# Performance work log

Measured on AMD Instinct MI355X. Metric: run time of the kernel, lower is better.

Reference implementation:

```python
import jax, jax.numpy as jnp
import numpy as np

B, S, E, H, FF = 4, 2048, 1024, 16, 4096
DK = E // H
EPS = 1e-5


def setup_inputs() -> dict:
    key = jax.random.key(0)
    ks = jax.random.split(key, 16)
    sc = 0.02
    return {
        "x": jax.random.normal(ks[0], (B, S, E), jnp.float32),
        "Wq": jax.random.normal(ks[1], (E, E), jnp.float32) * sc,
        "Wk": jax.random.normal(ks[2], (E, E), jnp.float32) * sc,
        "Wv": jax.random.normal(ks[3], (E, E), jnp.float32) * sc,
        "Wo": jax.random.normal(ks[4], (E, E), jnp.float32) * sc,
        "theta": jax.random.normal(ks[5], (DK,), jnp.float32),
        "Wcq": jax.random.normal(ks[6], (E, E), jnp.float32) * sc,
        "ln1_g": jnp.ones((E,), jnp.float32),
        "ln1_b": jnp.zeros((E,), jnp.float32),
        "W1": jax.random.normal(ks[7], (E, FF), jnp.float32) * sc,
        "b1": jnp.zeros((FF,), jnp.float32),
        "W2": jax.random.normal(ks[8], (FF, E), jnp.float32) * sc,
        "b2": jnp.zeros((E,), jnp.float32),
        "ln2_g": jnp.ones((E,), jnp.float32),
        "ln2_b": jnp.zeros((E,), jnp.float32),
    }


def _layernorm(x, g, b):
    mu = jnp.mean(x, axis=-1, keepdims=True)
    var = jnp.mean(jnp.square(x - mu), axis=-1, keepdims=True)
    return (x - mu) * jax.lax.rsqrt(var + EPS) * g + b


def reference(x, Wq, Wk, Wv, Wo, theta, Wcq, ln1_g, ln1_b, W1, b1, W2, b2, ln2_g, ln2_b):
    mix = 0.5
    # classical multi-head attention
    def heads(t):  # [B,S,E] -> [B,H,S,DK]
        return t.reshape(B, S, H, DK).transpose(0, 2, 1, 3)
    q = heads(x @ Wq)
    k = heads(x @ Wk)
    v = heads(x @ Wv)
    scores = jnp.einsum("bhqd,bhkd->bhqk", q, k) / jnp.sqrt(jnp.float32(DK))
    attn = jax.nn.softmax(scores, axis=-1)
    ctx = jnp.einsum("bhqk,bhkd->bhqd", attn, v)
    ctx = ctx.transpose(0, 2, 1, 3).reshape(B, S, E)
    classical = ctx @ Wo
    # quantum heads: RX(x)RX(theta)|0>, <Z> = cos(x + theta), same theta shared per head
    qh = jnp.cos(x.reshape(B, S, H, DK) + theta)  # broadcast over wires
    quantum = qh.reshape(B, S, E) @ Wcq
    attn_out = mix * classical + (1.0 - mix) * quantum
    x1 = _layernorm(x + attn_out, ln1_g, ln1_b)
    ffn = jax.nn.relu(x1 @ W1 + b1) @ W2 + b2
    return _layernorm(x1 + ffn, ln2_g, ln2_b)
```

## Files before the change

kernel.cpp:

```cpp
#include <hip/hip_runtime.h>
#include <hip/hip_bf16.h>

typedef __bf16 bf16_t;
typedef bf16_t bf16x8 __attribute__((ext_vector_type(8)));
typedef bf16_t bf16x4v __attribute__((ext_vector_type(4)));
typedef float f32x4 __attribute__((ext_vector_type(4)));
typedef unsigned u32x4 __attribute__((ext_vector_type(4)));

static constexpr int EE = 1024;
static constexpr int SS = 2048;
static constexpr int DK = 64;
static constexpr float QSCALE = 0.125f * 1.44269504f;

__device__ __forceinline__ void gload_lds16(const void* g, void* l) {
  __builtin_amdgcn_global_load_lds(
      (__attribute__((address_space(1))) void*)g,
      (__attribute__((address_space(3))) void*)l, 16, 0, 0);
}

__device__ __forceinline__ f32x4 mfma16(bf16x8 a, bf16x8 b, f32x4 c) {
  return __builtin_amdgcn_mfma_f32_16x16x32_bf16(a, b, c, 0, 0, 0);
}

template<int OFF>
__device__ __forceinline__ bf16x4v tr8(unsigned va) {
  bf16x4v d;
  asm volatile("ds_read_b64_tr_b16 %0, %1 offset:%c2"
               : "=v"(d) : "v"(va), "i"(OFF));
  return d;
}

__global__ void __launch_bounds__(256) prep_x_kernel(
    const float* __restrict__ x, const float* __restrict__ theta,
    bf16_t* __restrict__ xbf, bf16_t* __restrict__ A2)
{
  const long t = (long)blockIdx.x * 256 + threadIdx.x;
  const long e0 = t * 8;
  const int col = (int)(e0 & (EE - 1));
  const long row = e0 >> 10;
  const float4 v0 = *(const float4*)&x[e0];
  const float4 v1 = *(const float4*)&x[e0 + 4];
  float xs[8] = {v0.x, v0.y, v0.z, v0.w, v1.x, v1.y, v1.z, v1.w};
  const int d0 = col & (DK - 1);
  bf16x8 xb, qb;
#pragma unroll
  for (int j = 0; j < 8; ++j) {
    xb[j] = (bf16_t)xs[j];
    qb[j] = (bf16_t)__cosf(xs[j] + theta[d0 + j]);
  }
  *(bf16x8*)&xbf[e0] = xb;
  *(bf16x8*)&A2[row * 2048 + EE + col] = qb;
}

__global__ void __launch_bounds__(256) transpose_all_kernel(
    const float* __restrict__ Wq, const float* __restrict__ Wk,
    const float* __restrict__ Wv, const float* __restrict__ Wo,
    const float* __restrict__ Wcq, const float* __restrict__ W1,
    const float* __restrict__ W2,
    bf16_t* __restrict__ BtQKV, bf16_t* __restrict__ Bt2,
    bf16_t* __restrict__ BtW1, bf16_t* __restrict__ BtW2)
{
  const int bid = blockIdx.x;
  const float* src; bf16_t* dst; int N; long dstride, dcol0; int bx, by;
  if (bid < 5120) {
    const int seg = bid >> 10, r = bid & 1023;
    bx = r & 31; by = r >> 5; N = 1024;
    if      (seg == 0) { src = Wq;  dst = BtQKV;               dstride = 1024; dcol0 = 0; }
    else if (seg == 1) { src = Wk;  dst = BtQKV + 1024 * 1024; dstride = 1024; dcol0 = 0; }
    else if (seg == 2) { src = Wv;  dst = BtQKV + 2048 * 1024; dstride = 1024; dcol0 = 0; }
    else if (seg == 3) { src = Wo;  dst = Bt2;                 dstride = 2048; dcol0 = 0; }
    else               { src = Wcq; dst = Bt2;                 dstride = 2048; dcol0 = 1024; }
  } else if (bid < 9216) {
    const int r = bid - 5120;
    src = W1; dst = BtW1; N = 4096; dstride = 1024; dcol0 = 0;
    bx = r & 127; by = r >> 7;
  } else {
    const int r = bid - 9216;
    src = W2; dst = BtW2; N = 1024; dstride = 4096; dcol0 = 0;
    bx = r & 31; by = r >> 5;
  }
  __shared__ float tile[32][33];
  const int tx = threadIdx.x, ty = threadIdx.y;
  const long n0 = (long)bx * 32, k0 = (long)by * 32;
#pragma unroll
  for (int j = 0; j < 4; ++j)
    tile[ty + j * 8][tx] = src[(k0 + ty + j * 8) * N + n0 + tx];
  __syncthreads();
#pragma unroll
  for (int j = 0; j < 4; ++j)
    dst[(n0 + ty + j * 8) * dstride + dcol0 + k0 + tx] = (bf16_t)tile[tx][ty + j * 8];
}

template<int MODE, int TN>
__global__ void __launch_bounds__(512, 2) gemm256(
    const bf16_t* __restrict__ A, const bf16_t* __restrict__ Bt,
    void* __restrict__ C, int M, int N, int K,
    const float* __restrict__ aux1, const bf16_t* __restrict__ aux2)
{
  constexpr int MB  = (TN == 256) ? 8 : 4;
  constexpr int MBH = MB / 2;
  constexpr int NB  = 4;
  __shared__ bf16_t As[4][256 * 32];
  __shared__ bf16_t Bs[4][TN * 32];
  const int tid = threadIdx.x;
  const int lane = tid & 63, wid = tid >> 6;
  const int wr = (TN == 256) ? (wid >> 2) : (wid >> 1);
  const int wc = (TN == 256) ? (wid & 3) : (wid & 1);
  const int lr = lane & 15, lk = lane >> 4;
  const int gx = gridDim.x;
  const int nwg = gx * gridDim.y;
  const int bid = blockIdx.y * gx + blockIdx.x;
  const int swz = (bid & 7) * (nwg >> 3) + (bid >> 3);
  const long m0 = (long)(swz / gx) * 256;
  const long n0 = (long)(swz % gx) * TN;

  const int rql = lane >> 2;
  const int sl  = lane & 3;
  const int rA0 = wid * 32 + rql, rA1 = wid * 32 + 16 + rql;
  const bf16_t* sA0 = &A [(m0 + rA0) * K + 8 * (sl ^ ((rA0 >> 1) & 3))];
  const bf16_t* sA1 = &A [(m0 + rA1) * K + 8 * (sl ^ ((rA1 >> 1) & 3))];
  const int rB0 = (TN == 256) ? (wid * 32 + rql) : (wid * 16 + rql);
  const int rB1 = wid * 32 + 16 + rql;
  const bf16_t* sB0 = &Bt[(n0 + rB0) * K + 8 * (sl ^ ((rB0 >> 1) & 3))];
  const bf16_t* sB1 = &Bt[(n0 + rB1) * K + 8 * (sl ^ ((rB1 >> 1) & 3))];
  const int loA = wid * 1024;
  const int loB = (TN == 256) ? wid * 1024 : wid * 512;

  f32x4 acc[MB][NB] = {};
  const int NKT = K / 32;

  auto stA = [&](int t) {
    const int s = t & 3;
    gload_lds16(sA0 + (long)t * 32, &As[s][loA]);
    gload_lds16(sA1 + (long)t * 32, &As[s][loA + 512]);
  };
  auto stB = [&](int t) {
    const int s = t & 3;
    gload_lds16(sB0 + (long)t * 32, &Bs[s][loB]);
    if constexpr (TN == 256)
      gload_lds16(sB1 + (long)t * 32, &Bs[s][loB + 512]);
  };

  stA(0); stB(0); stA(1); stB(1); stA(2); stB(2);
  if constexpr (TN == 256) { asm volatile("s_waitcnt vmcnt(8)" ::: "memory"); }
  else                     { asm volatile("s_waitcnt vmcnt(6)" ::: "memory"); }
  __builtin_amdgcn_s_barrier();

  for (int t = 0; t < NKT; ++t) {
    const int s = t & 3;
    bf16x8 bfr[NB], af1[MBH], af2[MBH];
#pragma unroll
    for (int nb = 0; nb < NB; ++nb) {
      const int rw = wc * 64 + nb * 16 + lr;
      bfr[nb] = *(const bf16x8*)&Bs[s][rw * 32 + (lk ^ ((rw >> 1) & 3)) * 8];
    }
#pragma unroll
    for (int mb = 0; mb < MBH; ++mb) {
      const int rw = wr * (MB * 16) + mb * 16 + lr;
      af1[mb] = *(const bf16x8*)&As[s][rw * 32 + (lk ^ ((rw >> 1) & 3)) * 8];
    }
    __builtin_amdgcn_sched_barrier(0);
#pragma unroll
    for (int mb = 0; mb < MBH; ++mb) {
      const int rw = wr * (MB * 16) + (MBH + mb) * 16 + lr;
      af2[mb] = *(const bf16x8*)&As[s][rw * 32 + (lk ^ ((rw >> 1) & 3)) * 8];
    }
    if (t + 3 < NKT) { stA(t + 3); stB(t + 3); }
    if constexpr (MBH == 4) { asm volatile("s_waitcnt lgkmcnt(4)" ::: "memory"); }
    else                    { asm volatile("s_waitcnt lgkmcnt(2)" ::: "memory"); }
    __builtin_amdgcn_sched_barrier(0);
    __builtin_amdgcn_s_setprio(1);
#pragma unroll
    for (int mb = 0; mb < MBH; ++mb)
#pragma unroll
      for (int nb = 0; nb < NB; ++nb)
        acc[mb][nb] = mfma16(af1[mb], bfr[nb], acc[mb][nb]);
    __builtin_amdgcn_s_setprio(0);
    asm volatile("s_waitcnt lgkmcnt(0)" ::: "memory");
    __builtin_amdgcn_sched_barrier(0);
    __builtin_amdgcn_s_setprio(1);
#pragma unroll
    for (int mb = 0; mb < MBH; ++mb)
#pragma unroll
      for (int nb = 0; nb < NB; ++nb)
        acc[MBH + mb][nb] = mfma16(af2[mb], bfr[nb], acc[MBH + mb][nb]);
    __builtin_amdgcn_s_setprio(0);
    if (t + 3 < NKT) {
      if constexpr (TN == 256) { asm volatile("s_waitcnt vmcnt(8)" ::: "memory"); }
      else                     { asm volatile("s_waitcnt vmcnt(6)" ::: "memory"); }
    } else if (t + 3 == NKT) {
      if constexpr (TN == 256) { asm volatile("s_waitcnt vmcnt(4)" ::: "memory"); }
      else                     { asm volatile("s_waitcnt vmcnt(3)" ::: "memory"); }
    } else if (t + 2 == NKT) {
      asm volatile("s_waitcnt vmcnt(0)" ::: "memory");
    }
    __builtin_amdgcn_s_barrier();
  }

#pragma unroll
  for (int mb = 0; mb < MB; ++mb)
#pragma unroll
    for (int nb = 0; nb < NB; ++nb)
#pragma unroll
      for (int i = 0; i < 4; ++i) {
        const long r = m0 + wr * (MB * 16) + mb * 16 + lk * 4 + i;
        const long cc = n0 + wc * 64 + nb * 16 + lr;
        float v = acc[mb][nb][i];
        if constexpr (MODE == 0) {
          if (cc < 1024) v *= QSCALE;
          ((bf16_t*)C)[r * N + cc] = (bf16_t)v;
        } else if constexpr (MODE == 1) {
          ((float*)C)[r * N + cc] = 0.5f * v + aux1[r * N + cc];
        } else if constexpr (MODE == 2) {
          ((bf16_t*)C)[r * N + cc] = (bf16_t)fmaxf(v + aux1[cc], 0.0f);
        } else {
          ((float*)C)[r * N + cc] = v + aux1[cc] + (float)aux2[r * N + cc];
        }
      }
}

__global__ void __launch_bounds__(256, 2) attn_kernel(
    const bf16_t* __restrict__ QKV, bf16_t* __restrict__ Ctx)
{
  __shared__ bf16_t Ks[2][64 * 64];
  __shared__ bf16_t Vt[2][64 * 64];
  const int tid = threadIdx.x;
  const int lane = tid & 63, w = tid >> 6;
  const int lr = lane & 15, lk = lane >> 4;
  const int bh = blockIdx.x, b = bh >> 4, h = bh & 15;
  const long rowbase = (long)b * SS;
  const int q0 = blockIdx.y * 128;
  const int qcol = h * 64, kcol = EE + h * 64, vcol = 2 * EE + h * 64;
  constexpr int NT = SS / 64;

  bf16x8 qf[2][2];
#pragma unroll
  for (int mb = 0; mb < 2; ++mb)
#pragma unroll
    for (int ks = 0; ks < 2; ++ks)
      qf[mb][ks] = *(const bf16x8*)&QKV[
          (rowbase + q0 + w * 32 + mb * 16 + lr) * 3072 + qcol + ks * 32 + lk * 8];

  const int ksl = ((lane & 7) ^ ((lane >> 3) & 7)) * 8;
  const bf16_t* sK0 = &QKV[(rowbase + (2 * w + 0) * 8 + (lane >> 3)) * 3072 + kcol + ksl];
  const bf16_t* sK1 = &QKV[(rowbase + (2 * w + 1) * 8 + (lane >> 3)) * 3072 + kcol + ksl];
  const int vk = 4 * (lane >> 3) + ((lane >> 1) & 3);
  const int vd = 16 * w + 8 * (lane & 1);
  const bf16_t* sV0 = &QKV[(rowbase + vk) * 3072 + vcol + vd];
  const bf16_t* sV1 = &QKV[(rowbase + 32 + vk) * 3072 + vcol + vd];

  auto stage = [&](int t) {
    const int buf = t & 1;
    const long off = (long)t * 64 * 3072;
    gload_lds16(sK0 + off, &Ks[buf][(2 * w + 0) * 512]);
    gload_lds16(sK1 + off, &Ks[buf][(2 * w + 1) * 512]);
    gload_lds16(sV0 + off, &Vt[buf][(2 * w + 0) * 512]);
    gload_lds16(sV1 + off, &Vt[buf][(2 * w + 1) * 512]);
  };

  const unsigned vtr_base =
      (unsigned)(uintptr_t)(__attribute__((address_space(3))) void*)&Vt[0][0]
      + 2u * (unsigned)(lr + lk * 64);

  f32x4 oacc[2][4] = {};
  float lsum[2] = {0.0f, 0.0f};

  stage(0);

  for (int t = 0; t < NT; ++t) {
    const int buf = t & 1;
    __syncthreads();
    if (t + 1 < NT) stage(t + 1);

    bf16x8 kf[4][2];
#pragma unroll
    for (int nb = 0; nb < 4; ++nb)
#pragma unroll
      for (int ks = 0; ks < 2; ++ks)
        kf[nb][ks] = *(const bf16x8*)&Ks[buf][
            (nb * 16 + lr) * 64 + ((ks * 4 + lk) ^ (lr & 7)) * 8];

    f32x4 sacc[2][4] = {};
    __builtin_amdgcn_s_setprio(1);
#pragma unroll
    for (int mb = 0; mb < 2; ++mb)
#pragma unroll
      for (int nb = 0; nb < 4; ++nb)
#pragma unroll
        for (int ks = 0; ks < 2; ++ks)
          sacc[mb][nb] = mfma16(kf[nb][ks], qf[mb][ks], sacc[mb][nb]);
    __builtin_amdgcn_s_setprio(0);

    const unsigned va = vtr_base + (unsigned)buf * 8192u;
    bf16x4v vlo[4][2], vhi[4][2];
    vlo[0][0] = tr8<   0>(va);  vhi[0][0] = tr8< 512>(va);
    vlo[0][1] = tr8<1024>(va);  vhi[0][1] = tr8<1536>(va);
    vlo[1][0] = tr8<2048>(va);  vhi[1][0] = tr8<2560>(va);
    vlo[1][1] = tr8<3072>(va);  vhi[1][1] = tr8<3584>(va);
    vlo[2][0] = tr8<4096>(va);  vhi[2][0] = tr8<4608>(va);
    vlo[2][1] = tr8<5120>(va);  vhi[2][1] = tr8<5632>(va);
    vlo[3][0] = tr8<6144>(va);  vhi[3][0] = tr8<6656>(va);
    vlo[3][1] = tr8<7168>(va);  vhi[3][1] = tr8<7680>(va);

#pragma unroll
    for (int mb = 0; mb < 2; ++mb) {
      float psum = 0.0f;
      u32x4 pk[2];
#pragma unroll
      for (int nb = 0; nb < 4; ++nb)
#pragma unroll
        for (int p = 0; p < 2; ++p) {
          const float a = __builtin_amdgcn_exp2f(sacc[mb][nb][2 * p]);
          const float bb = __builtin_amdgcn_exp2f(sacc[mb][nb][2 * p + 1]);
          psum += a + bb;
          unsigned pr;
          asm("v_cvt_pk_bf16_f32 %0, %1, %2" : "=v"(pr) : "v"(a), "v"(bb));
          pk[nb >> 1][(nb & 1) * 2 + p] = pr;
        }
      lsum[mb] += psum;
      const bf16x8 pf0 = __builtin_bit_cast(bf16x8, pk[0]);
      const bf16x8 pf1 = __builtin_bit_cast(bf16x8, pk[1]);
      asm volatile("s_waitcnt lgkmcnt(0)" ::: "memory");
      __builtin_amdgcn_sched_barrier(0);
      __builtin_amdgcn_s_setprio(1);
#pragma unroll
      for (int nb = 0; nb < 4; ++nb)
#pragma unroll
        for (int ks = 0; ks < 2; ++ks) {
          const bf16x8 vf = __builtin_shufflevector(
              vlo[nb][ks], vhi[nb][ks], 0, 1, 2, 3, 4, 5, 6, 7);
          oacc[mb][nb] = mfma16(ks ? pf1 : pf0, vf, oacc[mb][nb]);
        }
      __builtin_amdgcn_s_setprio(0);
    }
  }

#pragma unroll
  for (int mb = 0; mb < 2; ++mb) {
    float l = lsum[mb];
    l += __shfl_xor(l, 16);
    l += __shfl_xor(l, 32);
    float li[4];
#pragma unroll
    for (int i = 0; i < 4; ++i) li[i] = 1.0f / __shfl(l, lk * 4 + i);
#pragma unroll
    for (int nb = 0; nb < 4; ++nb)
#pragma unroll
      for (int i = 0; i < 4; ++i) {
        const long r = rowbase + q0 + w * 32 + mb * 16 + lk * 4 + i;
        Ctx[r * 2048 + h * 64 + nb * 16 + lr] = (bf16_t)(oacc[mb][nb][i] * li[i]);
      }
  }
}

__device__ __forceinline__ void ln_reduce(const float4& v, int tid,
                                          float& mu, float& rs) {
  float s = v.x + v.y + v.z + v.w;
  float ss = v.x * v.x + v.y * v.y + v.z * v.z + v.w * v.w;
#pragma unroll
  for (int off = 1; off < 64; off <<= 1) {
    s += __shfl_xor(s, off);
    ss += __shfl_xor(ss, off);
  }
  __shared__ float wsum[4], wsq[4];
  if ((tid & 63) == 0) { wsum[tid >> 6] = s; wsq[tid >> 6] = ss; }
  __syncthreads();
  s = wsum[0] + wsum[1] + wsum[2] + wsum[3];
  ss = wsq[0] + wsq[1] + wsq[2] + wsq[3];
  mu = s * (1.0f / EE);
  rs = rsqrtf(ss * (1.0f / EE) - mu * mu + 1e-5f);
}

__global__ void __launch_bounds__(256) ln_bf16_kernel(
    const float* __restrict__ pre, const float* __restrict__ g,
    const float* __restrict__ bt, bf16_t* __restrict__ out)
{
  const int r = blockIdx.x, tid = threadIdx.x;
  const long base = (long)r * EE + tid * 4;
  const float4 v = *(const float4*)&pre[base];
  float mu, rs;
  ln_reduce(v, tid, mu, rs);
  const float4 gv = *(const float4*)&g[tid * 4];
  const float4 bv = *(const float4*)&bt[tid * 4];
  bf16x4v o;
  o[0] = (bf16_t)((v.x - mu) * rs * gv.x + bv.x);
  o[1] = (bf16_t)((v.y - mu) * rs * gv.y + bv.y);
  o[2] = (bf16_t)((v.z - mu) * rs * gv.z + bv.z);
  o[3] = (bf16_t)((v.w - mu) * rs * gv.w + bv.w);
  *(bf16x4v*)&out[base] = o;
}

__global__ void __launch_bounds__(256) ln_f32_kernel(
    const float* __restrict__ pre, const float* __restrict__ g,
    const float* __restrict__ bt, float* __restrict__ out)
{
  const int r = blockIdx.x, tid = threadIdx.x;
  const long base = (long)r * EE + tid * 4;
  const float4 v = *(const float4*)&pre[base];
  float mu, rs;
  ln_reduce(v, tid, mu, rs);
  const float4 gv = *(const float4*)&g[tid * 4];
  const float4 bv = *(const float4*)&bt[tid * 4];
  float4 o;
  o.x = (v.x - mu) * rs * gv.x + bv.x;
  o.y = (v.y - mu) * rs * gv.y + bv.y;
  o.z = (v.z - mu) * rs * gv.z + bv.z;
  o.w = (v.w - mu) * rs * gv.w + bv.w;
  *(float4*)&out[base] = o;
}

extern "C" void kernel_launch(void* const* d_in, const int* in_sizes, int n_in,
                              void* d_out, int out_size, void* d_ws, size_t ws_size,
                              hipStream_t stream)
{
  (void)in_sizes; (void)n_in; (void)out_size; (void)ws_size;
  const float* x     = (const float*)d_in[0];
  const float* Wq    = (const float*)d_in[1];
  const float* Wk    = (const float*)d_in[2];
  const float* Wv    = (const float*)d_in[3];
  const float* Wo    = (const float*)d_in[4];
  const float* theta = (const float*)d_in[5];
  const float* Wcq   = (const float*)d_in[6];
  const float* ln1g  = (const float*)d_in[7];
  const float* ln1b  = (const float*)d_in[8];
  const float* W1    = (const float*)d_in[9];
  const float* b1    = (const float*)d_in[10];
  const float* W2    = (const float*)d_in[11];
  const float* b2    = (const float*)d_in[12];
  const float* ln2g  = (const float*)d_in[13];
  const float* ln2b  = (const float*)d_in[14];

  char* ws = (char*)d_ws;
  const size_t MB = 1ull << 20;
  bf16_t* xbf    = (bf16_t*)(ws + 0);
  bf16_t* QKV    = (bf16_t*)(ws + 16 * MB);
  float*  preLN1 = (float*)(ws + 16 * MB);
  bf16_t* A2     = (bf16_t*)(ws + 64 * MB);
  float*  preLN2 = (float*)(ws + 64 * MB);
  bf16_t* H1     = (bf16_t*)(ws + 96 * MB);
  bf16_t* BtQKV  = (bf16_t*)(ws + 160 * MB);
  bf16_t* Bt2    = (bf16_t*)(ws + 166 * MB);
  bf16_t* BtW1   = (bf16_t*)(ws + 170 * MB);
  bf16_t* BtW2   = (bf16_t*)(ws + 178 * MB);

  prep_x_kernel<<<4096, 256, 0, stream>>>(x, theta, xbf, A2);
  transpose_all_kernel<<<13312, dim3(32, 8), 0, stream>>>(
      Wq, Wk, Wv, Wo, Wcq, W1, W2, BtQKV, Bt2, BtW1, BtW2);

  gemm256<0, 128><<<dim3(24, 32), 512, 0, stream>>>(xbf, BtQKV, QKV, 8192, 3072, 1024, nullptr, nullptr);
  attn_kernel<<<dim3(64, 16), 256, 0, stream>>>(QKV, A2);
  gemm256<1, 128><<<dim3(8, 32), 512, 0, stream>>>(A2, Bt2, preLN1, 8192, 1024, 2048, x, nullptr);
  ln_bf16_kernel<<<8192, 256, 0, stream>>>(preLN1, ln1g, ln1b, xbf);
  gemm256<2, 256><<<dim3(16, 32), 512, 0, stream>>>(xbf, BtW1, H1, 8192, 4096, 1024, b1, nullptr);
  gemm256<3, 128><<<dim3(8, 32), 512, 0, stream>>>(H1, BtW2, preLN2, 8192, 1024, 4096, b2, xbf);
  ln_f32_kernel<<<8192, 256, 0, stream>>>(preLN2, ln2g, ln2b, (float*)d_out);
}
```

Baseline: 413.0 us.

## Add 256x256 ping-pong pipelined GEMM for QKV and FFN1 projections

Adds a new gemm8p kernel with 256x256 tiles and a K-step of 64. It double-buffers A and B halves in LDS and interleaves global-to-LDS loads, LDS fragment reads and MFMA blocks under fine-grained waitcnt, barriers and setprio scheduling. The QKV projection and the first FFN GEMM now use it in place of gemm256, which drops the old MODE 0 and 2 epilogues from gemm256. The aim is better overlap of memory traffic with matrix math and more reuse per tile. The cost is higher register and LDS pressure (128 KB of LDS per block) and fragile hand scheduling.

New measurement: 429.4 us. +4.0%, slower.

```diff
diff --git a/kernel.cpp b/kernel.cpp
--- a/kernel.cpp
+++ b/kernel.cpp
@@ -91,6 +91,124 @@
     dst[(n0 + ty + j * 8) * dstride + dcol0 + k0 + tx] = (bf16_t)tile[tx][ty + j * 8];
 }
 
+#define G8_VM6 asm volatile("s_waitcnt vmcnt(6)" ::: "memory")
+#define G8_LG(n) asm volatile("s_waitcnt lgkmcnt(" #n ")" ::: "memory")
+#define G8_BAR __builtin_amdgcn_s_barrier()
+#define G8_SCB __builtin_amdgcn_sched_barrier(0)
+#define G8_P1 __builtin_amdgcn_s_setprio(1)
+#define G8_P0 __builtin_amdgcn_s_setprio(0)
+#define G8_SA(bb, h, tt) do { \
+    gload_lds16(bA + (long)((h) * 128) * K + (long)(tt) * 64, \
+                &AsF[((bb) * 2 + (h)) * 8192 + wid * 512]); \
+    gload_lds16(bA + (long)((h) * 128 + 64) * K + (long)(tt) * 64, \
+                &AsF[((bb) * 2 + (h)) * 8192 + 4096 + wid * 512]); } while (0)
+#define G8_SB(bb, h, tt) do { \
+    gload_lds16(bB + (long)((h) * 128) * K + (long)(tt) * 64, \
+                &BsF[((bb) * 2 + (h)) * 8192 + wid * 512]); \
+    gload_lds16(bB + (long)((h) * 128 + 64) * K + (long)(tt) * 64, \
+                &BsF[((bb) * 2 + (h)) * 8192 + 4096 + wid * 512]); } while (0)
+#define G8_RA(bb, mh) do { \
+    _Pragma("unroll") for (int mb2 = 0; mb2 < 4; ++mb2) \
+    _Pragma("unroll") for (int ks = 0; ks < 2; ++ks) { \
+      const int r_ = (mh) * 64 + mb2 * 16 + lr; \
+      fa[mh][mb2][ks] = *(const bf16x8*)&AsF[ \
+          ((bb) * 2 + wr) * 8192 + r_ * 64 + (((ks << 2) | lk) ^ (r_ & 7)) * 8]; } } while (0)
+#define G8_RB(bb, nh) do { \
+    _Pragma("unroll") for (int nb2 = 0; nb2 < 2; ++nb2) \
+    _Pragma("unroll") for (int ks = 0; ks < 2; ++ks) { \
+      const int rw_ = wc * 64 + (nh) * 32 + nb2 * 16 + lr; \
+      fb[nh][nb2][ks] = *(const bf16x8*)&BsF[ \
+          ((bb) * 2 + (wc >> 1)) * 8192 + (rw_ & 127) * 64 + (((ks << 2) | lk) ^ (rw_ & 7)) * 8]; } } while (0)
+#define G8_MM(mh, nh) do { \
+    _Pragma("unroll") for (int mb2 = 0; mb2 < 4; ++mb2) \
+    _Pragma("unroll") for (int nb2 = 0; nb2 < 2; ++nb2) \
+    _Pragma("unroll") for (int ks = 0; ks < 2; ++ks) \
+      acc[(mh) * 4 + mb2][(nh) * 2 + nb2] = \
+          mfma16(fa[mh][mb2][ks], fb[nh][nb2][ks], acc[(mh) * 4 + mb2][(nh) * 2 + nb2]); } while (0)
+
+template<int MODE>
+__global__ void __launch_bounds__(512, 2) gemm8p(
+    const bf16_t* __restrict__ A, const bf16_t* __restrict__ Bt,
+    void* __restrict__ C, int M, int N, int K, const float* __restrict__ aux1)
+{
+  __shared__ bf16_t AsF[32768];
+  __shared__ bf16_t BsF[32768];
+  const int tid = threadIdx.x;
+  const int lane = tid & 63, wid = tid >> 6;
+  const int wr = wid >> 2, wc = wid & 3;
+  const int lr = lane & 15, lk = lane >> 4;
+  const int gx = gridDim.x;
+  const int nwg = gx * gridDim.y;
+  const int bid = blockIdx.y * gx + blockIdx.x;
+  const int swz = (bid & 7) * (nwg >> 3) + (bid >> 3);
+  const long m0 = (long)(swz / gx) * 256;
+  const long n0 = (long)(swz % gx) * 256;
+
+  const int strow = tid >> 3, stslot = tid & 7;
+  const int scol = 8 * (stslot ^ (strow & 7));
+  const bf16_t* bA = &A [(m0 + strow) * K + scol];
+  const bf16_t* bB = &Bt[(n0 + strow) * K + scol];
+
+  f32x4 acc[8][4] = {};
+  bf16x8 fa[2][4][2], fb[2][2][2];
+  const int NKT = K / 64, NIT = NKT / 2;
+
+  G8_SB(0, 0, 0); G8_SB(0, 1, 0);
+  G8_SA(0, 0, 0); G8_SA(0, 1, 0);
+  G8_SB(1, 0, 1); G8_SB(1, 1, 1);
+  G8_VM6; G8_BAR;
+  G8_RA(0, 0); G8_RB(0, 0);
+
+  for (int itr = 0; itr < NIT; ++itr) {
+    const int t = 2 * itr;
+    G8_SA(1, 0, t + 1); G8_VM6; G8_BAR;
+    G8_RB(0, 1);
+    G8_LG(4); G8_SCB; G8_P1; G8_MM(0, 0); G8_P0; G8_BAR;
+    G8_SA(1, 1, t + 1); G8_BAR;
+    G8_RA(0, 1);
+    G8_LG(8); G8_SCB; G8_P1; G8_MM(0, 1); G8_P0; G8_BAR;
+    if (t + 2 < NKT) G8_SB(0, 0, t + 2);
+    G8_BAR;
+    G8_LG(0); G8_SCB; G8_P1; G8_MM(1, 0); G8_P0; G8_BAR;
+    if (t + 2 < NKT) G8_SB(0, 1, t + 2);
+    G8_VM6; G8_BAR;
+    G8_RA(1, 0); G8_RB(1, 0);
+    G8_LG(12); G8_SCB; G8_P1; G8_MM(1, 1); G8_P0; G8_BAR;
+    if (t + 2 < NKT) G8_SA(0, 0, t + 2);
+    G8_VM6; G8_BAR;
+    G8_RB(1, 1);
+    G8_LG(4); G8_SCB; G8_P1; G8_MM(0, 0); G8_P0; G8_BAR;
+    if (t + 2 < NKT) G8_SA(0, 1, t + 2);
+    G8_BAR;
+    G8_RA(1, 1);
+    G8_LG(8); G8_SCB; G8_P1; G8_MM(0, 1); G8_P0; G8_BAR;
+    if (t + 3 < NKT) G8_SB(1, 0, t + 3);
+    G8_BAR;
+    G8_LG(0); G8_SCB; G8_P1; G8_MM(1, 0); G8_P0; G8_BAR;
+    if (t + 3 < NKT) G8_SB(1, 1, t + 3);
+    G8_VM6; G8_BAR;
+    if (itr + 1 < NIT) { G8_RA(0, 0); G8_RB(0, 0); }
+    G8_LG(12); G8_SCB; G8_P1; G8_MM(1, 1); G8_P0; G8_BAR;
+  }
+
+#pragma unroll
+  for (int mb = 0; mb < 8; ++mb)
+#pragma unroll
+    for (int nb = 0; nb < 4; ++nb)
+#pragma unroll
+      for (int i = 0; i < 4; ++i) {
+        const long r = m0 + wr * 128 + (mb >> 2) * 64 + (mb & 3) * 16 + lk * 4 + i;
+        const long cc = n0 + wc * 64 + (nb >> 1) * 32 + (nb & 1) * 16 + lr;
+        float v = acc[mb][nb][i];
+        if constexpr (MODE == 0) {
+          if (cc < 1024) v *= QSCALE;
+          ((bf16_t*)C)[r * N + cc] = (bf16_t)v;
+        } else {
+          ((bf16_t*)C)[r * N + cc] = (bf16_t)fmaxf(v + aux1[cc], 0.0f);
+        }
+      }
+}
+
 template<int MODE, int TN>
 __global__ void __launch_bounds__(512, 2) gemm256(
     const bf16_t* __restrict__ A, const bf16_t* __restrict__ Bt,
@@ -206,13 +324,8 @@
         const long r = m0 + wr * (MB * 16) + mb * 16 + lk * 4 + i;
         const long cc = n0 + wc * 64 + nb * 16 + lr;
         float v = acc[mb][nb][i];
-        if constexpr (MODE == 0) {
-          if (cc < 1024) v *= QSCALE;
-          ((bf16_t*)C)[r * N + cc] = (bf16_t)v;
-        } else if constexpr (MODE == 1) {
+        if constexpr (MODE == 1) {
           ((float*)C)[r * N + cc] = 0.5f * v + aux1[r * N + cc];
-        } else if constexpr (MODE == 2) {
-          ((bf16_t*)C)[r * N + cc] = (bf16_t)fmaxf(v + aux1[cc], 0.0f);
         } else {
           ((float*)C)[r * N + cc] = v + aux1[cc] + (float)aux2[r * N + cc];
         }
@@ -447,11 +560,11 @@
   transpose_all_kernel<<<13312, dim3(32, 8), 0, stream>>>(
       Wq, Wk, Wv, Wo, Wcq, W1, W2, BtQKV, Bt2, BtW1, BtW2);
 
-  gemm256<0, 128><<<dim3(24, 32), 512, 0, stream>>>(xbf, BtQKV, QKV, 8192, 3072, 1024, nullptr, nullptr);
+  gemm8p<0><<<dim3(12, 32), 512, 0, stream>>>(xbf, BtQKV, QKV, 8192, 3072, 1024, nullptr);
   attn_kernel<<<dim3(64, 16), 256, 0, stream>>>(QKV, A2);
   gemm256<1, 128><<<dim3(8, 32), 512, 0, stream>>>(A2, Bt2, preLN1, 8192, 1024, 2048, x, nullptr);
   ln_bf16_kernel<<<8192, 256, 0, stream>>>(preLN1, ln1g, ln1b, xbf);
-  gemm256<2, 256><<<dim3(16, 32), 512, 0, stream>>>(xbf, BtW1, H1, 8192, 4096, 1024, b1, nullptr);
+  gemm8p<2><<<dim3(16, 32), 512, 0, stream>>>(xbf, BtW1, H1, 8192, 4096, 1024, b1);
   gemm256<3, 128><<<dim3(8, 32), 512, 0, stream>>>(H1, BtW2, preLN2, 8192, 1024, 4096, b2, xbf);
   ln_f32_kernel<<<8192, 256, 0, stream>>>(preLN2, ln2g, ln2b, (float*)d_out);
 }
```
